# Optimization experiments

Hardware: AMD Instinct MI355X
Metric: run time of the kernel (lower is better)

The kernel has to match this reference:

```python
import jax, jax.numpy as jnp
import numpy as np

NUM_HEADS = 8

def setup_inputs() -> dict:
    key = jax.random.key(0)
    ks = jax.random.split(key, 6)
    B, S, D, K = 2, 2048, 512, 64
    x = jax.random.normal(ks[0], (B, S, D), dtype=jnp.float32)
    routes = jax.random.randint(ks[1], (S, K), 0, S, dtype=jnp.int32)
    distances = jax.random.uniform(ks[2], (S, S), dtype=jnp.float32)
    W_in = jax.random.normal(ks[3], (D, D), dtype=jnp.float32) * (1.0 / np.sqrt(D))
    W_out = jax.random.normal(ks[4], (D, D), dtype=jnp.float32) * (1.0 / np.sqrt(D))
    b_out = jnp.zeros((D,), dtype=jnp.float32)
    return {"x": x, "routes": routes, "distances": distances,
            "W_in": W_in, "W_out": W_out, "b_out": b_out}

def reference(x, routes, distances, W_in, W_out, b_out):
    # x: [B,S,D]; routes: [S,K] int gather table; distances: [S,S]
    B, S, D = x.shape
    H = NUM_HEADS
    hd = D // H
    K = routes.shape[1]
    # in_proj (torch Linear, no bias): y = x @ W^T
    h = jnp.einsum('bsd,ed->bse', x, W_in).reshape(B, S, H, hd)
    # gather fusion windows via precomputed routes: [B,S,K,H,hd]
    gathered = h[:, routes]
    # weighted fusion: weights from precomputed Cantor distance matrix
    d = jnp.take_along_axis(distances, routes.astype(jnp.int32), axis=1)  # [S,K]
    w = jax.nn.softmax(-d, axis=-1)  # normalized fusion weights
    fused = jnp.einsum('sk,bskhd->bshd', w, gathered)  # [B,S,H,hd]
    fused = fused.reshape(B, S, D)
    # out_proj + residual (dropout is identity in eval)
    out = jnp.einsum('bsd,ed->bse', fused, W_out) + b_out
    return out + x
```

## Files before the change

### kernel.cpp

```cpp
#include <hip/hip_runtime.h>
#include <hip/hip_bf16.h>

#define S_DIM 2048
#define D_DIM 512
#define B_DIM 2
#define K_RT  64
#define M_DIM 4096

#define GBM 64
#define GBN 64
#define GBK 64

typedef __attribute__((ext_vector_type(8))) short short8;
typedef __attribute__((ext_vector_type(4))) float f32x4;
typedef unsigned int u32;
#define AS1 __attribute__((address_space(1)))
#define AS3 __attribute__((address_space(3)))

static __device__ __forceinline__ float bf16lo_to_f(unsigned u) {
    union { unsigned u; float f; } c; c.u = u << 16; return c.f;
}
static __device__ __forceinline__ float bf16hi_to_f(unsigned u) {
    union { unsigned u; float f; } c; c.u = u & 0xffff0000u; return c.f;
}
static __device__ __forceinline__ unsigned short f_to_bf16(float f) {
    union { float f; unsigned u; } c; c.f = f;
    unsigned u = c.u;
    u += 0x7fffu + ((u >> 16) & 1u);
    return (unsigned short)(u >> 16);
}
static __device__ __forceinline__ unsigned pk2(float a, float b) {
    return (unsigned)f_to_bf16(a) | ((unsigned)f_to_bf16(b) << 16);
}

__global__ __launch_bounds__(256) void prep_cast(
    const float* __restrict__ x, const float* __restrict__ Wi, const float* __restrict__ Wo,
    unsigned short* __restrict__ xb, unsigned short* __restrict__ wib,
    unsigned short* __restrict__ wob)
{
    const int g = blockIdx.x * 256 + threadIdx.x;
    const int NX = M_DIM * D_DIM / 4;
    const int NW = D_DIM * D_DIM / 4;
    const float* src; unsigned short* dst; int off;
    if (g < NX)           { src = x;  dst = xb;  off = g; }
    else if (g < NX + NW) { src = Wi; dst = wib; off = g - NX; }
    else                  { src = Wo; dst = wob; off = g - NX - NW; }
    const float4 v = ((const float4*)src)[off];
    ushort4 o;
    o.x = f_to_bf16(v.x); o.y = f_to_bf16(v.y);
    o.z = f_to_bf16(v.z); o.w = f_to_bf16(v.w);
    ((ushort4*)dst)[off] = o;
}

template<bool OUTF32>
__global__ __launch_bounds__(256) void gemm_bt(
    const unsigned short* __restrict__ A,
    const unsigned short* __restrict__ B,
    void* __restrict__ Cv,
    const float* __restrict__ bias, const float* __restrict__ residual)
{
    __shared__ unsigned short As[4][GBM * 32];
    __shared__ unsigned short Bs[4][GBN * 32];

    const int N = D_DIM, K = D_DIM;
    const int tid  = threadIdx.x;
    const int lane = tid & 63;
    const int wv   = tid >> 6;
    const int bid  = blockIdx.x;
    const int within = bid >> 3;
    const int m0 = ((bid & 7) * 8 + (within >> 3)) * GBM;
    const int n0 = (within & 7) * GBN;
    const int wm = (wv & 1) * 32;
    const int wn = (wv >> 1) * 32;

    const int srow  = wv * 16 + (lane >> 2);
    const int skoff = (lane & 3) * 8;
    const unsigned short* Arow = A + (size_t)(m0 + srow) * K + skoff;
    const unsigned short* Brow = B + (size_t)(n0 + srow) * K + skoff;

    const int mi = lane & 15;
    const int kg = lane >> 4;

    f32x4 acc[2][2] = {};

#define STAGE(buf, k0) do {                                                              \
    __builtin_amdgcn_global_load_lds((const AS1 u32*)(Arow + (k0)),                      \
                                     (AS3 u32*)(As[(buf)*2 + 0] + wv * 512), 16, 0, 0);  \
    __builtin_amdgcn_global_load_lds((const AS1 u32*)(Arow + (k0) + 32),                 \
                                     (AS3 u32*)(As[(buf)*2 + 1] + wv * 512), 16, 0, 0);  \
    __builtin_amdgcn_global_load_lds((const AS1 u32*)(Brow + (k0)),                      \
                                     (AS3 u32*)(Bs[(buf)*2 + 0] + wv * 512), 16, 0, 0);  \
    __builtin_amdgcn_global_load_lds((const AS1 u32*)(Brow + (k0) + 32),                 \
                                     (AS3 u32*)(Bs[(buf)*2 + 1] + wv * 512), 16, 0, 0);  \
} while (0)

    STAGE(0, 0);
    __syncthreads();

    #pragma unroll
    for (int t = 0; t < K / GBK; ++t) {
        const int cur = t & 1;
        if (t + 1 < K / GBK) STAGE(cur ^ 1, (t + 1) * GBK);
        #pragma unroll
        for (int kh = 0; kh < 2; ++kh) {
            short8 af0 = *(const short8*)(As[cur*2 + kh] + (wm +      mi) * 32 + kg * 8);
            short8 af1 = *(const short8*)(As[cur*2 + kh] + (wm + 16 + mi) * 32 + kg * 8);
            short8 bf0 = *(const short8*)(Bs[cur*2 + kh] + (wn +      mi) * 32 + kg * 8);
            short8 bf1 = *(const short8*)(Bs[cur*2 + kh] + (wn + 16 + mi) * 32 + kg * 8);

            acc[0][0] = __builtin_amdgcn_mfma_f32_16x16x32_bf16(af0, bf0, acc[0][0], 0, 0, 0);
            acc[0][1] = __builtin_amdgcn_mfma_f32_16x16x32_bf16(af0, bf1, acc[0][1], 0, 0, 0);
            acc[1][0] = __builtin_amdgcn_mfma_f32_16x16x32_bf16(af1, bf0, acc[1][0], 0, 0, 0);
            acc[1][1] = __builtin_amdgcn_mfma_f32_16x16x32_bf16(af1, bf1, acc[1][1], 0, 0, 0);
        }
        __syncthreads();
    }
#undef STAGE

    const int rb  = (lane >> 4) * 4;
    const int col = lane & 15;
    #pragma unroll
    for (int i = 0; i < 2; ++i) {
        #pragma unroll
        for (int j = 0; j < 2; ++j) {
            #pragma unroll
            for (int r = 0; r < 4; ++r) {
                const int m = m0 + wm + i * 16 + rb + r;
                const int n = n0 + wn + j * 16 + col;
                const float v = acc[i][j][r];
                if (OUTF32) {
                    ((float*)Cv)[(size_t)m * N + n] = v + bias[n] + residual[(size_t)m * N + n];
                } else {
                    ((unsigned short*)Cv)[(size_t)m * N + n] = f_to_bf16(v);
                }
            }
        }
    }
}

__global__ __launch_bounds__(256, 4) void fuse_gather(
    const unsigned short* __restrict__ h, const int* __restrict__ routes,
    const float* __restrict__ distances, unsigned short* __restrict__ fused)
{
    const int tid  = threadIdx.x;
    const int lane = tid & 63;
    const int wv   = tid >> 6;
    const int bx   = blockIdx.x;
    const int b    = bx & 1;
    const int s    = (bx >> 1) * 4 + wv;

    const int rt = routes[s * K_RT + lane];
    const float v = -distances[(size_t)s * S_DIM + rt];
    float mx = v;
    #pragma unroll
    for (int off = 32; off >= 1; off >>= 1) mx = fmaxf(mx, __shfl_xor(mx, off, 64));
    const float e = __expf(v - mx);
    float sum = e;
    #pragma unroll
    for (int off = 32; off >= 1; off >>= 1) sum += __shfl_xor(sum, off, 64);
    const float wl = e / sum;

    const unsigned short* hb = h + (size_t)b * S_DIM * D_DIM;
    float acc0[8] = {}, acc1[8] = {};
    #pragma unroll
    for (int k = 0; k < 32; ++k) {
        const int   rk0 = __builtin_amdgcn_readlane(rt, k);
        const int   rk1 = __builtin_amdgcn_readlane(rt, k + 32);
        const float wk0 = __int_as_float(__builtin_amdgcn_readlane(__float_as_int(wl), k));
        const float wk1 = __int_as_float(__builtin_amdgcn_readlane(__float_as_int(wl), k + 32));
        const uint4 p0 = *(const uint4*)(hb + (size_t)rk0 * D_DIM + lane * 8);
        const uint4 p1 = *(const uint4*)(hb + (size_t)rk1 * D_DIM + lane * 8);
        acc0[0] = fmaf(wk0, bf16lo_to_f(p0.x), acc0[0]);
        acc0[1] = fmaf(wk0, bf16hi_to_f(p0.x), acc0[1]);
        acc0[2] = fmaf(wk0, bf16lo_to_f(p0.y), acc0[2]);
        acc0[3] = fmaf(wk0, bf16hi_to_f(p0.y), acc0[3]);
        acc0[4] = fmaf(wk0, bf16lo_to_f(p0.z), acc0[4]);
        acc0[5] = fmaf(wk0, bf16hi_to_f(p0.z), acc0[5]);
        acc0[6] = fmaf(wk0, bf16lo_to_f(p0.w), acc0[6]);
        acc0[7] = fmaf(wk0, bf16hi_to_f(p0.w), acc0[7]);
        acc1[0] = fmaf(wk1, bf16lo_to_f(p1.x), acc1[0]);
        acc1[1] = fmaf(wk1, bf16hi_to_f(p1.x), acc1[1]);
        acc1[2] = fmaf(wk1, bf16lo_to_f(p1.y), acc1[2]);
        acc1[3] = fmaf(wk1, bf16hi_to_f(p1.y), acc1[3]);
        acc1[4] = fmaf(wk1, bf16lo_to_f(p1.z), acc1[4]);
        acc1[5] = fmaf(wk1, bf16hi_to_f(p1.z), acc1[5]);
        acc1[6] = fmaf(wk1, bf16lo_to_f(p1.w), acc1[6]);
        acc1[7] = fmaf(wk1, bf16hi_to_f(p1.w), acc1[7]);
    }
    uint4 o;
    o.x = pk2(acc0[0] + acc1[0], acc0[1] + acc1[1]);
    o.y = pk2(acc0[2] + acc1[2], acc0[3] + acc1[3]);
    o.z = pk2(acc0[4] + acc1[4], acc0[5] + acc1[5]);
    o.w = pk2(acc0[6] + acc1[6], acc0[7] + acc1[7]);
    *(uint4*)(fused + ((size_t)b * S_DIM + s) * D_DIM + lane * 8) = o;
}

extern "C" void kernel_launch(void* const* d_in, const int* in_sizes, int n_in,
                              void* d_out, int out_size, void* d_ws, size_t ws_size,
                              hipStream_t stream) {
    const float* x         = (const float*)d_in[0];
    const int*   routes    = (const int*)  d_in[1];
    const float* distances = (const float*)d_in[2];
    const float* W_in      = (const float*)d_in[3];
    const float* W_out     = (const float*)d_in[4];
    const float* b_out     = (const float*)d_in[5];
    float* out = (float*)d_out;

    unsigned short* xb  = (unsigned short*)d_ws;
    unsigned short* wib = xb  + (size_t)M_DIM * D_DIM;
    unsigned short* wob = wib + (size_t)D_DIM * D_DIM;
    unsigned short* hb  = wob + (size_t)D_DIM * D_DIM;
    unsigned short* fb  = hb  + (size_t)M_DIM * D_DIM;

    prep_cast<<<2560, 256, 0, stream>>>(x, W_in, W_out, xb, wib, wob);
    gemm_bt<false><<<512, 256, 0, stream>>>(xb, wib, hb, nullptr, nullptr);
    fuse_gather<<<dim3(1024), 256, 0, stream>>>(hb, routes, distances, fb);
    gemm_bt<true><<<512, 256, 0, stream>>>(fb, wob, out, b_out, x);
}
```

Before: 116.6 us.

## Fuse fp32-to-bf16 casts into GEMM tile loads and drop prep kernel

Removes the separate prep_cast kernel. The GEMMs now load fp32 x and weights directly through registers, convert them to bf16 and write them to LDS, with register prefetch of the next k-tile overlapping the MFMA work. This saves one launch and the round trip of writing and reading the bf16 copies. In exchange, the async global_load_lds DMA for those operands becomes a register-staged path that costs more VGPRs and adds conversion ALU work inside the main loop, and the weights are reconverted by every block.

```diff
diff --git a/kernel.cpp b/kernel.cpp
--- a/kernel.cpp
+++ b/kernel.cpp
@@ -1,9 +1,7 @@
 #include <hip/hip_runtime.h>
-#include <hip/hip_bf16.h>
 
 #define S_DIM 2048
 #define D_DIM 512
-#define B_DIM 2
 #define K_RT  64
 #define M_DIM 4096
 
@@ -32,30 +30,17 @@
 static __device__ __forceinline__ unsigned pk2(float a, float b) {
     return (unsigned)f_to_bf16(a) | ((unsigned)f_to_bf16(b) << 16);
 }
-
-__global__ __launch_bounds__(256) void prep_cast(
-    const float* __restrict__ x, const float* __restrict__ Wi, const float* __restrict__ Wo,
-    unsigned short* __restrict__ xb, unsigned short* __restrict__ wib,
-    unsigned short* __restrict__ wob)
-{
-    const int g = blockIdx.x * 256 + threadIdx.x;
-    const int NX = M_DIM * D_DIM / 4;
-    const int NW = D_DIM * D_DIM / 4;
-    const float* src; unsigned short* dst; int off;
-    if (g < NX)           { src = x;  dst = xb;  off = g; }
-    else if (g < NX + NW) { src = Wi; dst = wib; off = g - NX; }
-    else                  { src = Wo; dst = wob; off = g - NX - NW; }
-    const float4 v = ((const float4*)src)[off];
-    ushort4 o;
-    o.x = f_to_bf16(v.x); o.y = f_to_bf16(v.y);
-    o.z = f_to_bf16(v.z); o.w = f_to_bf16(v.w);
-    ((ushort4*)dst)[off] = o;
-}
-
-template<bool OUTF32>
+static __device__ __forceinline__ short8 pack8(float4 a, float4 b) {
+    union { short8 s; unsigned u[4]; } r;
+    r.u[0] = pk2(a.x, a.y); r.u[1] = pk2(a.z, a.w);
+    r.u[2] = pk2(b.x, b.y); r.u[3] = pk2(b.z, b.w);
+    return r.s;
+}
+
+template<bool OUTF32, bool AF32>
 __global__ __launch_bounds__(256) void gemm_bt(
-    const unsigned short* __restrict__ A,
-    const unsigned short* __restrict__ B,
+    const void* __restrict__ Av,
+    const float* __restrict__ Bf,
     void* __restrict__ Cv,
     const float* __restrict__ bias, const float* __restrict__ residual)
 {
@@ -73,34 +58,55 @@
     const int wm = (wv & 1) * 32;
     const int wn = (wv >> 1) * 32;
 
-    const int srow  = wv * 16 + (lane >> 2);
-    const int skoff = (lane & 3) * 8;
-    const unsigned short* Arow = A + (size_t)(m0 + srow) * K + skoff;
-    const unsigned short* Brow = B + (size_t)(n0 + srow) * K + skoff;
+    const int srow = wv * 16 + (lane >> 2);
+    const int c    = lane & 3;
+    const int kh_w = c >> 1;
+    const int kb_w = (c & 1) * 16;
+    const float* Bsrc = Bf + (size_t)(n0 + srow) * K + c * 16;
+    const float* Asrc = AF32 ? ((const float*)Av + (size_t)(m0 + srow) * K + c * 16) : nullptr;
+    const unsigned short* Arow16 = AF32 ? nullptr :
+        ((const unsigned short*)Av + (size_t)(m0 + srow) * K + (lane & 3) * 8);
 
     const int mi = lane & 15;
     const int kg = lane >> 4;
 
     f32x4 acc[2][2] = {};
 
-#define STAGE(buf, k0) do {                                                              \
-    __builtin_amdgcn_global_load_lds((const AS1 u32*)(Arow + (k0)),                      \
+#define LOAD4(dst, src, k0) do {                       \
+    dst[0] = *(const float4*)((src) + (k0));           \
+    dst[1] = *(const float4*)((src) + (k0) + 4);       \
+    dst[2] = *(const float4*)((src) + (k0) + 8);       \
+    dst[3] = *(const float4*)((src) + (k0) + 12);      \
+} while (0)
+#define WR8(panelArr, buf, regs) do {                                                        \
+    *(short8*)(panelArr[(buf)*2 + kh_w] + srow * 32 + kb_w)     = pack8(regs[0], regs[1]);   \
+    *(short8*)(panelArr[(buf)*2 + kh_w] + srow * 32 + kb_w + 8) = pack8(regs[2], regs[3]);   \
+} while (0)
+#define DMA_A(buf, k0) do {                                                              \
+    __builtin_amdgcn_global_load_lds((const AS1 u32*)(Arow16 + (k0)),                    \
                                      (AS3 u32*)(As[(buf)*2 + 0] + wv * 512), 16, 0, 0);  \
-    __builtin_amdgcn_global_load_lds((const AS1 u32*)(Arow + (k0) + 32),                 \
+    __builtin_amdgcn_global_load_lds((const AS1 u32*)(Arow16 + (k0) + 32),               \
                                      (AS3 u32*)(As[(buf)*2 + 1] + wv * 512), 16, 0, 0);  \
-    __builtin_amdgcn_global_load_lds((const AS1 u32*)(Brow + (k0)),                      \
-                                     (AS3 u32*)(Bs[(buf)*2 + 0] + wv * 512), 16, 0, 0);  \
-    __builtin_amdgcn_global_load_lds((const AS1 u32*)(Brow + (k0) + 32),                 \
-                                     (AS3 u32*)(Bs[(buf)*2 + 1] + wv * 512), 16, 0, 0);  \
 } while (0)
 
-    STAGE(0, 0);
-    __syncthreads();
+    {
+        float4 ar[4], br[4];
+        if constexpr (AF32) LOAD4(ar, Asrc, 0); else DMA_A(0, 0);
+        LOAD4(br, Bsrc, 0);
+        if constexpr (AF32) WR8(As, 0, ar);
+        WR8(Bs, 0, br);
+        __syncthreads();
+    }
 
     #pragma unroll
     for (int t = 0; t < K / GBK; ++t) {
         const int cur = t & 1;
-        if (t + 1 < K / GBK) STAGE(cur ^ 1, (t + 1) * GBK);
+        float4 ar[4], br[4];
+        if (t + 1 < K / GBK) {
+            const int k0n = (t + 1) * GBK;
+            if constexpr (AF32) LOAD4(ar, Asrc, k0n); else DMA_A(cur ^ 1, k0n);
+            LOAD4(br, Bsrc, k0n);
+        }
         #pragma unroll
         for (int kh = 0; kh < 2; ++kh) {
             short8 af0 = *(const short8*)(As[cur*2 + kh] + (wm +      mi) * 32 + kg * 8);
@@ -113,9 +119,15 @@
             acc[1][0] = __builtin_amdgcn_mfma_f32_16x16x32_bf16(af1, bf0, acc[1][0], 0, 0, 0);
             acc[1][1] = __builtin_amdgcn_mfma_f32_16x16x32_bf16(af1, bf1, acc[1][1], 0, 0, 0);
         }
+        if (t + 1 < K / GBK) {
+            if constexpr (AF32) WR8(As, cur ^ 1, ar);
+            WR8(Bs, cur ^ 1, br);
+        }
         __syncthreads();
     }
-#undef STAGE
+#undef LOAD4
+#undef WR8
+#undef DMA_A
 
     const int rb  = (lane >> 4) * 4;
     const int col = lane & 15;
@@ -206,14 +218,10 @@
     const float* b_out     = (const float*)d_in[5];
     float* out = (float*)d_out;
 
-    unsigned short* xb  = (unsigned short*)d_ws;
-    unsigned short* wib = xb  + (size_t)M_DIM * D_DIM;
-    unsigned short* wob = wib + (size_t)D_DIM * D_DIM;
-    unsigned short* hb  = wob + (size_t)D_DIM * D_DIM;
-    unsigned short* fb  = hb  + (size_t)M_DIM * D_DIM;
-
-    prep_cast<<<2560, 256, 0, stream>>>(x, W_in, W_out, xb, wib, wob);
-    gemm_bt<false><<<512, 256, 0, stream>>>(xb, wib, hb, nullptr, nullptr);
+    unsigned short* hb = (unsigned short*)d_ws;
+    unsigned short* fb = hb + (size_t)M_DIM * D_DIM;
+
+    gemm_bt<false, true><<<512, 256, 0, stream>>>((const void*)x, W_in, hb, nullptr, nullptr);
     fuse_gather<<<dim3(1024), 256, 0, stream>>>(hb, routes, distances, fb);
-    gemm_bt<true><<<512, 256, 0, stream>>>(fb, wob, out, b_out, x);
-}
+    gemm_bt<true, false><<<512, 256, 0, stream>>>((const void*)fb, W_out, out, b_out, x);
+}
```

Result: no change. 117.6 us (+0.8%).
